# Kernel optimization log

Hardware: AMD Instinct MI355X
Metric: run time of the kernel (lower is better)

## Reference

```python
import jax, jax.numpy as jnp
import numpy as np
import math

D_MODEL = 1024
NHEAD = 16
D_HEAD = D_MODEL // NHEAD
TAU = 300.0
DELTA = 5.0 * 60.0  # delta_minutes -> seconds


def setup_inputs() -> dict:
    key = jax.random.key(0)
    ks = jax.random.split(key, 10)
    B, M = 4, 2048
    H = jax.random.normal(ks[0], (B, M, D_MODEL), dtype=jnp.float32)
    patch_mask = jax.random.randint(ks[1], (B, M), 0, 2).astype(jnp.int32)
    s = 1.0 / math.sqrt(D_MODEL)
    Wq = jax.random.normal(ks[2], (D_MODEL, D_MODEL), dtype=jnp.float32) * s
    bq = jnp.zeros((D_MODEL,), dtype=jnp.float32)
    Wk = jax.random.normal(ks[3], (D_MODEL, D_MODEL), dtype=jnp.float32) * s
    bk = jnp.zeros((D_MODEL,), dtype=jnp.float32)
    Wv = jax.random.normal(ks[4], (D_MODEL, D_MODEL), dtype=jnp.float32) * s
    bv = jnp.zeros((D_MODEL,), dtype=jnp.float32)
    Wo = jax.random.normal(ks[5], (D_MODEL, D_MODEL), dtype=jnp.float32) * s
    bo = jnp.zeros((D_MODEL,), dtype=jnp.float32)
    return {"H": H, "patch_mask": patch_mask, "Wq": Wq, "bq": bq,
            "Wk": Wk, "bk": bk, "Wv": Wv, "bv": bv, "Wo": Wo, "bo": bo}


def _time_bias(M):
    idx = jnp.arange(M)
    dist = jnp.abs(idx[:, None] - idx[None, :]).astype(jnp.float32) * DELTA
    w = jnp.exp(-dist / max(TAU, 1e-6))
    return jnp.log(w + 1e-12)  # (M, M)


def reference(H, patch_mask, Wq, bq, Wk, bk, Wv, bv, Wo, bo):
    B, M, D = H.shape
    nh, dh = NHEAD, D_HEAD
    # projections -> (B, nh, M, dh)
    q = (H @ Wq.T + bq).reshape(B, M, nh, dh).transpose(0, 2, 1, 3)
    k = (H @ Wk.T + bk).reshape(B, M, nh, dh).transpose(0, 2, 1, 3)
    v = (H @ Wv.T + bv).reshape(B, M, nh, dh).transpose(0, 2, 1, 3)
    attn = jnp.einsum('bhqd,bhkd->bhqk', q, k) / math.sqrt(dh)
    attn = attn + _time_bias(M)[None, None, :, :]
    key_pad = patch_mask <= 0  # (B, M)
    attn = jnp.where(key_pad[:, None, None, :], -1e9, attn)
    A = jax.nn.softmax(attn, axis=-1)
    out = jnp.einsum('bhqk,bhkd->bhqd', A, v)
    out = out.transpose(0, 2, 1, 3).reshape(B, M, D)
    out = out @ Wo.T + bo
    out = out * patch_mask[:, :, None].astype(out.dtype)
    return out
```

## Files before the change

### kernel.cpp

```cpp
#include <hip/hip_runtime.h>
#include <stdint.h>

typedef short short8 __attribute__((ext_vector_type(8)));
typedef float f32x4 __attribute__((ext_vector_type(4)));

#define B_    4
#define M_    2048
#define D_    1024
#define NH_   16
#define DH_   64
#define LOG2E 1.44269504f

__device__ __forceinline__ short f2bf(float f) {
  union { float f; uint32_t u; } v; v.f = f;
  uint32_t r = (v.u + 0x7fffu + ((v.u >> 16) & 1u)) >> 16;
  return (short)r;
}

__device__ __forceinline__ void gl_lds16(const void* g, void* l) {
  __builtin_amdgcn_global_load_lds(
      (__attribute__((address_space(1))) void*)(g),
      (__attribute__((address_space(3))) void*)(l),
      16, 0, 0);
}

__device__ __forceinline__ f32x4 mfma16(short8 a, short8 b, f32x4 c) {
  return __builtin_amdgcn_mfma_f32_16x16x32_bf16(a, b, c, 0, 0, 0);
}

__global__ __launch_bounds__(256) void cvt_all(const float* __restrict__ H,
                                               const float* __restrict__ s0,
                                               const float* __restrict__ s1,
                                               const float* __restrict__ s2,
                                               const float* __restrict__ s3,
                                               short* __restrict__ dH,
                                               short* __restrict__ d0,
                                               short* __restrict__ d1,
                                               short* __restrict__ d2,
                                               short* __restrict__ d3) {
  const int bidx = blockIdx.x;
  const float* src;
  short* dst;
  int i;
  if (bidx < 8192) {
    src = H; dst = dH; i = bidx * 256 + threadIdx.x;
  } else {
    const int y = (bidx - 8192) >> 10;
    src = (y == 0) ? s0 : (y == 1) ? s1 : (y == 2) ? s2 : s3;
    dst = (y == 0) ? d0 : (y == 1) ? d1 : (y == 2) ? d2 : d3;
    i = ((bidx - 8192) & 1023) * 256 + threadIdx.x;
  }
  float4 v = ((const float4*)src)[i];
  short4 o;
  o.x = f2bf(v.x); o.y = f2bf(v.y); o.z = f2bf(v.z); o.w = f2bf(v.w);
  ((short4*)dst)[i] = o;
}

__global__ __launch_bounds__(256, 3) void gemm_qkv(const short* __restrict__ A,
                                                   const short* __restrict__ Wqb,
                                                   const short* __restrict__ Wkb,
                                                   const short* __restrict__ Wvb,
                                                   const float* __restrict__ bq,
                                                   const float* __restrict__ bk,
                                                   const float* __restrict__ bv,
                                                   short* __restrict__ Qo,
                                                   short* __restrict__ Ko,
                                                   short* __restrict__ Vo) {
  __shared__ char smem_raw[34816];
  short* Abuf = (short*)smem_raw;
  short* Bbuf = (short*)smem_raw + 4096;

  const int L = blockIdx.x + 8 * (blockIdx.y + 64 * blockIdx.z);
  const int xcd = L & 7;
  const int s = L >> 3;
  const int m_local = s & 7;
  const int nz = s >> 3;
  const int nt = nz & 7, z = nz >> 3;
  const int m0 = (xcd * 8 + m_local) * 128;
  const int n0 = nt * 128;

  const short* Bt = (z == 0) ? Wqb : (z == 1) ? Wkb : Wvb;
  const float* bias = (z == 0) ? bq : (z == 1) ? bk : bv;
  const float scale = (z == 0) ? 0.125f : 1.0f;

  const int tid = threadIdx.x;
  const int w = tid >> 6, l = tid & 63;
  const int q4 = l >> 4, c = l & 15;
  const int wr = w >> 1, wc = w & 1;

  f32x4 acc[4][4] = {};
  const int arow = (l >> 2);
  const int acol = (l & 3) * 8;

  for (int kk = 0; kk < 32; ++kk) {
    const int k0 = kk * 32;
#pragma unroll
    for (int st = 0; st < 2; ++st) {
      const int chunk = w * 2 + st;
      gl_lds16(A + (size_t)(m0 + chunk * 16 + arow) * 1024 + k0 + acol,
               Abuf + chunk * 512);
      gl_lds16(Bt + (size_t)(n0 + chunk * 16 + arow) * 1024 + k0 + acol,
               Bbuf + chunk * 512);
    }
    __syncthreads();
    short8 af[4], bfr[4];
#pragma unroll
    for (int i = 0; i < 4; ++i)
      af[i] = *(const short8*)(Abuf + (wr * 64 + i * 16 + c) * 32 + q4 * 8);
#pragma unroll
    for (int j = 0; j < 4; ++j)
      bfr[j] = *(const short8*)(Bbuf + (wc * 64 + j * 16 + c) * 32 + q4 * 8);
#pragma unroll
    for (int i = 0; i < 4; ++i)
#pragma unroll
      for (int j = 0; j < 4; ++j)
        acc[i][j] = mfma16(af[i], bfr[j], acc[i][j]);
    __syncthreads();
  }

  if (z < 2) {
    short* Cb = (short*)smem_raw;
    short* out = (z == 0) ? Qo : Ko;
#pragma unroll
    for (int j = 0; j < 4; ++j) {
      const float bvv = bias[n0 + wc * 64 + j * 16 + c];
#pragma unroll
      for (int i = 0; i < 4; ++i)
#pragma unroll
        for (int r = 0; r < 4; ++r)
          Cb[(wr * 64 + i * 16 + q4 * 4 + r) * 136 + wc * 64 + j * 16 + c] =
              f2bf((acc[i][j][r] + bvv) * scale);
    }
    __syncthreads();
#pragma unroll
    for (int p = 0; p < 8; ++p) {
      const int g = p * 256 + tid;
      const int row = g >> 4, seg = g & 15;
      *(short8*)(out + (size_t)(m0 + row) * 1024 + n0 + seg * 8) =
          *(const short8*)(Cb + row * 136 + seg * 8);
    }
  } else {
    short* Cb = (short*)smem_raw;
#pragma unroll
    for (int j = 0; j < 4; ++j) {
      const float bvv = bias[n0 + wc * 64 + j * 16 + c];
#pragma unroll
      for (int i = 0; i < 4; ++i) {
        short4 pk;
        pk.x = f2bf(acc[i][j][0] + bvv);
        pk.y = f2bf(acc[i][j][1] + bvv);
        pk.z = f2bf(acc[i][j][2] + bvv);
        pk.w = f2bf(acc[i][j][3] + bvv);
        *(short4*)(Cb + (wc * 64 + j * 16 + c) * 136 + wr * 64 + i * 16 + q4 * 4) = pk;
      }
    }
    __syncthreads();
    const int bb = m0 >> 11;
    const int tokb = m0 & 2047;
#pragma unroll
    for (int p = 0; p < 8; ++p) {
      const int g = p * 256 + tid;
      const int col = g >> 4, rseg = g & 15;
      const int colg = n0 + col;
      const int hh = colg >> 6, dd = colg & 63;
      *(short8*)(Vo + ((size_t)(bb * NH_ + hh) * DH_ + dd) * M_ + tokb + rseg * 8) =
          *(const short8*)(Cb + col * 136 + rseg * 8);
    }
  }
}

__global__ __launch_bounds__(256, 3) void gemm_oproj(const short* __restrict__ A,
                                                     const short* __restrict__ Bt,
                                                     const float* __restrict__ bias,
                                                     const int* __restrict__ pmask,
                                                     float* __restrict__ outp) {
  __shared__ char smem_raw[34816];
  short* Abuf = (short*)smem_raw;
  short* Bbuf = (short*)smem_raw + 4096;

  const int L = blockIdx.x + 8 * blockIdx.y;
  const int xcd = L & 7;
  const int s = L >> 3;
  const int m_local = s & 7;
  const int nt = s >> 3;
  const int m0 = (xcd * 8 + m_local) * 128;
  const int n0 = nt * 128;

  const int tid = threadIdx.x;
  const int w = tid >> 6, l = tid & 63;
  const int q4 = l >> 4, c = l & 15;
  const int wr = w >> 1, wc = w & 1;

  f32x4 acc[4][4] = {};
  const int arow = (l >> 2);
  const int acol = (l & 3) * 8;

  for (int kk = 0; kk < 32; ++kk) {
    const int k0 = kk * 32;
#pragma unroll
    for (int st = 0; st < 2; ++st) {
      const int chunk = w * 2 + st;
      gl_lds16(A + (size_t)(m0 + chunk * 16 + arow) * 1024 + k0 + acol,
               Abuf + chunk * 512);
      gl_lds16(Bt + (size_t)(n0 + chunk * 16 + arow) * 1024 + k0 + acol,
               Bbuf + chunk * 512);
    }
    __syncthreads();
    short8 af[4], bfr[4];
#pragma unroll
    for (int i = 0; i < 4; ++i)
      af[i] = *(const short8*)(Abuf + (wr * 64 + i * 16 + c) * 32 + q4 * 8);
#pragma unroll
    for (int j = 0; j < 4; ++j)
      bfr[j] = *(const short8*)(Bbuf + (wc * 64 + j * 16 + c) * 32 + q4 * 8);
#pragma unroll
    for (int i = 0; i < 4; ++i)
#pragma unroll
      for (int j = 0; j < 4; ++j)
        acc[i][j] = mfma16(af[i], bfr[j], acc[i][j]);
    __syncthreads();
  }

  float* Cf = (float*)smem_raw;
#pragma unroll
  for (int half = 0; half < 2; ++half) {
    __syncthreads();
    if (wr == half) {
#pragma unroll
      for (int j = 0; j < 4; ++j) {
        const float bvv = bias[n0 + wc * 64 + j * 16 + c];
#pragma unroll
        for (int i = 0; i < 4; ++i)
#pragma unroll
          for (int r = 0; r < 4; ++r)
            Cf[(i * 16 + q4 * 4 + r) * 132 + wc * 64 + j * 16 + c] =
                acc[i][j][r] + bvv;
      }
    }
    __syncthreads();
#pragma unroll
    for (int p = 0; p < 8; ++p) {
      const int g = p * 256 + tid;
      const int row = g >> 5, seg = g & 31;
      const int rowg = m0 + half * 64 + row;
      const float mmv = (pmask[rowg] > 0) ? 1.0f : 0.0f;
      float4 v = *(const float4*)(Cf + row * 132 + seg * 4);
      v.x *= mmv; v.y *= mmv; v.z *= mmv; v.w *= mmv;
      *(float4*)(outp + (size_t)rowg * 1024 + n0 + seg * 4) = v;
    }
  }
}

__global__ __launch_bounds__(256) void attn_kernel(const short* __restrict__ Qb,
                                                   const short* __restrict__ Kb,
                                                   const short* __restrict__ Vtb,
                                                   const int* __restrict__ pmask,
                                                   short* __restrict__ Attb) {
  __shared__ char smem[20480];
  short* Qs = (short*)smem;
  short* Ks = (short*)(smem + 8192);
  short* Vs = (short*)(smem + 12288);
  short* Ps = (short*)(smem + 16384);

  const int tid = threadIdx.x;
  const int w = tid >> 6, l = tid & 63;
  const int q4 = l >> 4, c = l & 15;
  const int qt = blockIdx.x, h = blockIdx.y, b = blockIdx.z;
  const short* Qbase = Qb + (size_t)(b * M_ + qt * 64) * D_ + h * DH_;
  const short* Kbase = Kb + (size_t)(b * M_) * D_ + h * DH_;
  const short* Vbase = Vtb + (size_t)(b * NH_ + h) * DH_ * M_;
  const int qrow0 = qt * 64 + w * 16;

  const int jt0 = max(0, 2 * qt - 2);
  const int jt1 = min(M_ / 32 - 1, 2 * qt + 3);

#pragma unroll
  for (int p = 0; p < 2; ++p) {
    const int u = p * 256 + tid;
    const int kh = u >> 8, row = (u >> 2) & 63, ch = u & 3;
    gl_lds16(Qbase + (size_t)row * D_ + kh * 32 + ch * 8, (char*)Qs + u * 16);
  }
  {
    const int j0 = jt0 * 32;
    const int kh = tid >> 7, krow = (tid >> 2) & 31, ch = tid & 3;
    gl_lds16(Kbase + (size_t)(j0 + krow) * D_ + kh * 32 + ch * 8, (char*)Ks + tid * 16);
    const int vrow = tid >> 2;
    gl_lds16(Vbase + (size_t)vrow * M_ + j0 + ch * 8, (char*)Vs + tid * 16);
  }
  __syncthreads();

  short8 aq0 = *(const short8*)(Qs + (w * 16 + c) * 32 + q4 * 8);
  short8 aq1 = *(const short8*)(Qs + 2048 + (w * 16 + c) * 32 + q4 * 8);

  f32x4 o[4] = {};
  float lrun[4] = {0.f, 0.f, 0.f, 0.f};
  short* Pw = Ps + w * 512;

  for (int jt = jt0; jt <= jt1; ++jt) {
    const int j0 = jt * 32;
    short8 b00 = *(const short8*)(Ks + c * 32 + q4 * 8);
    short8 b10 = *(const short8*)(Ks + 1024 + c * 32 + q4 * 8);
    short8 b01 = *(const short8*)(Ks + (16 + c) * 32 + q4 * 8);
    short8 b11 = *(const short8*)(Ks + 1024 + (16 + c) * 32 + q4 * 8);
    f32x4 s0 = {}, s1 = {};
    s0 = mfma16(aq0, b00, s0);
    s0 = mfma16(aq1, b10, s0);
    s1 = mfma16(aq0, b01, s1);
    s1 = mfma16(aq1, b11, s1);

    const float w0m = (pmask[b * M_ + j0 + c] > 0) ? 1.f : 0.f;
    const float w1m = (pmask[b * M_ + j0 + 16 + c] > 0) ? 1.f : 0.f;

#pragma unroll
    for (int r = 0; r < 4; ++r) {
      const int qr = qrow0 + q4 * 4 + r;
      const float d0 = fminf(fabsf((float)(qr - (j0 + c))), 28.0f);
      const float d1 = fminf(fabsf((float)(qr - (j0 + 16 + c))), 28.0f);
      const float p0 = exp2f((s0[r] - d0) * LOG2E) * w0m;
      const float p1 = exp2f((s1[r] - d1) * LOG2E) * w1m;
      Pw[(q4 * 4 + r) * 32 + c] = f2bf(p0);
      Pw[(q4 * 4 + r) * 32 + 16 + c] = f2bf(p1);
      lrun[r] += p0 + p1;
    }
    short8 pa = *(const short8*)(Pw + c * 32 + q4 * 8);
#pragma unroll
    for (int f = 0; f < 4; ++f) {
      short8 bv = *(const short8*)(Vs + (f * 16 + c) * 32 + q4 * 8);
      o[f] = mfma16(pa, bv, o[f]);
    }

    if (jt < jt1) {
      __syncthreads();
      const int j0n = j0 + 32;
      const int kh = tid >> 7, krow = (tid >> 2) & 31, ch = tid & 3;
      gl_lds16(Kbase + (size_t)(j0n + krow) * D_ + kh * 32 + ch * 8,
               (char*)Ks + tid * 16);
      const int vrow = tid >> 2;
      gl_lds16(Vbase + (size_t)vrow * M_ + j0n + ch * 8, (char*)Vs + tid * 16);
      __syncthreads();
    }
  }

#pragma unroll
  for (int r = 0; r < 4; ++r) {
#pragma unroll
    for (int off = 1; off < 16; off <<= 1)
      lrun[r] += __shfl_xor(lrun[r], off);
  }

  __syncthreads();
  short* Cb = (short*)(smem + 8192);
#pragma unroll
  for (int r = 0; r < 4; ++r) {
    const float inv = 1.0f / lrun[r];
#pragma unroll
    for (int f = 0; f < 4; ++f)
      Cb[(w * 16 + q4 * 4 + r) * 72 + f * 16 + c] = f2bf(o[f][r] * inv);
  }
  __syncthreads();
#pragma unroll
  for (int p = 0; p < 2; ++p) {
    const int u = p * 256 + tid;
    const int row = u >> 3, seg = u & 7;
    *(short8*)(Attb + (size_t)(b * M_ + qt * 64 + row) * D_ + h * DH_ + seg * 8) =
        *(const short8*)(Cb + row * 72 + seg * 8);
  }
}

extern "C" void kernel_launch(void* const* d_in, const int* in_sizes, int n_in,
                              void* d_out, int out_size, void* d_ws, size_t ws_size,
                              hipStream_t stream) {
  const float* H     = (const float*)d_in[0];
  const int*   pmask = (const int*)d_in[1];
  const float* Wq    = (const float*)d_in[2];
  const float* bq    = (const float*)d_in[3];
  const float* Wk    = (const float*)d_in[4];
  const float* bk    = (const float*)d_in[5];
  const float* Wv    = (const float*)d_in[6];
  const float* bv    = (const float*)d_in[7];
  const float* Wo    = (const float*)d_in[8];
  const float* bo    = (const float*)d_in[9];
  float* out = (float*)d_out;
  char* ws = (char*)d_ws;

  short* Hb   = (short*)(ws);
  short* Attb = (short*)(ws);
  short* Wqb  = (short*)(ws + (16u << 20));
  short* Wkb  = (short*)(ws + (18u << 20));
  short* Wvb  = (short*)(ws + (20u << 20));
  short* Wob  = (short*)(ws + (22u << 20));
  short* Qb   = (short*)(ws + (24u << 20));
  short* Kb2  = (short*)(ws + (40u << 20));
  short* Vtb  = (short*)(ws + (56u << 20));

  cvt_all<<<8192 + 4096, 256, 0, stream>>>(H, Wq, Wk, Wv, Wo,
                                           Hb, Wqb, Wkb, Wvb, Wob);

  dim3 gq(8, 64, 3);
  gemm_qkv<<<gq, 256, 0, stream>>>(Hb, Wqb, Wkb, Wvb, bq, bk, bv, Qb, Kb2, Vtb);

  attn_kernel<<<dim3(M_ / 64, NH_, B_), 256, 0, stream>>>(Qb, Kb2, Vtb, pmask, Attb);

  gemm_oproj<<<dim3(8, 64), 256, 0, stream>>>(Attb, Wob, bo, pmask, out);
}
```

Before: 222.4 us.

## Double-buffer K/V in attention and narrow output-projection tiles to 128x64

The attention kernel now ping-pongs between two K/V LDS buffers. It prefetches the next tile before computing on the current one and needs only one barrier per iteration. Q fragments are loaded straight from global memory into registers instead of going through LDS. The output-projection GEMM switches from 128x128 to 128x64 tiles, which doubles the block count to 1024 and drops the occupancy hint. This is meant to improve load balance across CUs, at the cost of lower per-block reuse of the A tile.

```diff
diff --git a/kernel.cpp b/kernel.cpp
--- a/kernel.cpp
+++ b/kernel.cpp
@@ -169,29 +169,29 @@
   }
 }
 
-__global__ __launch_bounds__(256, 3) void gemm_oproj(const short* __restrict__ A,
-                                                     const short* __restrict__ Bt,
-                                                     const float* __restrict__ bias,
-                                                     const int* __restrict__ pmask,
-                                                     float* __restrict__ outp) {
-  __shared__ char smem_raw[34816];
-  short* Abuf = (short*)smem_raw;
-  short* Bbuf = (short*)smem_raw + 4096;
-
-  const int L = blockIdx.x + 8 * blockIdx.y;
+__global__ __launch_bounds__(256) void gemm_oproj(const short* __restrict__ A,
+                                                  const short* __restrict__ Bt,
+                                                  const float* __restrict__ bias,
+                                                  const int* __restrict__ pmask,
+                                                  float* __restrict__ outp) {
+  __shared__ char smem[17408];
+  short* Abuf = (short*)smem;
+  short* Bbuf = (short*)(smem + 8192);
+
+  const int L = blockIdx.x + 16 * blockIdx.y;
   const int xcd = L & 7;
   const int s = L >> 3;
   const int m_local = s & 7;
   const int nt = s >> 3;
   const int m0 = (xcd * 8 + m_local) * 128;
-  const int n0 = nt * 128;
+  const int n0 = nt * 64;
 
   const int tid = threadIdx.x;
   const int w = tid >> 6, l = tid & 63;
   const int q4 = l >> 4, c = l & 15;
   const int wr = w >> 1, wc = w & 1;
 
-  f32x4 acc[4][4] = {};
+  f32x4 acc[4][2] = {};
   const int arow = (l >> 2);
   const int acol = (l & 3) * 8;
 
@@ -202,49 +202,49 @@
       const int chunk = w * 2 + st;
       gl_lds16(A + (size_t)(m0 + chunk * 16 + arow) * 1024 + k0 + acol,
                Abuf + chunk * 512);
-      gl_lds16(Bt + (size_t)(n0 + chunk * 16 + arow) * 1024 + k0 + acol,
-               Bbuf + chunk * 512);
-    }
-    __syncthreads();
-    short8 af[4], bfr[4];
+    }
+    gl_lds16(Bt + (size_t)(n0 + w * 16 + arow) * 1024 + k0 + acol,
+             Bbuf + w * 512);
+    __syncthreads();
+    short8 af[4], bfr[2];
 #pragma unroll
     for (int i = 0; i < 4; ++i)
       af[i] = *(const short8*)(Abuf + (wr * 64 + i * 16 + c) * 32 + q4 * 8);
 #pragma unroll
-    for (int j = 0; j < 4; ++j)
-      bfr[j] = *(const short8*)(Bbuf + (wc * 64 + j * 16 + c) * 32 + q4 * 8);
+    for (int j = 0; j < 2; ++j)
+      bfr[j] = *(const short8*)(Bbuf + (wc * 32 + j * 16 + c) * 32 + q4 * 8);
 #pragma unroll
     for (int i = 0; i < 4; ++i)
 #pragma unroll
-      for (int j = 0; j < 4; ++j)
+      for (int j = 0; j < 2; ++j)
         acc[i][j] = mfma16(af[i], bfr[j], acc[i][j]);
     __syncthreads();
   }
 
-  float* Cf = (float*)smem_raw;
+  float* Cf = (float*)smem;
 #pragma unroll
   for (int half = 0; half < 2; ++half) {
     __syncthreads();
     if (wr == half) {
 #pragma unroll
-      for (int j = 0; j < 4; ++j) {
-        const float bvv = bias[n0 + wc * 64 + j * 16 + c];
+      for (int j = 0; j < 2; ++j) {
+        const float bvv = bias[n0 + wc * 32 + j * 16 + c];
 #pragma unroll
         for (int i = 0; i < 4; ++i)
 #pragma unroll
           for (int r = 0; r < 4; ++r)
-            Cf[(i * 16 + q4 * 4 + r) * 132 + wc * 64 + j * 16 + c] =
+            Cf[(i * 16 + q4 * 4 + r) * 68 + wc * 32 + j * 16 + c] =
                 acc[i][j][r] + bvv;
       }
     }
     __syncthreads();
 #pragma unroll
-    for (int p = 0; p < 8; ++p) {
+    for (int p = 0; p < 4; ++p) {
       const int g = p * 256 + tid;
-      const int row = g >> 5, seg = g & 31;
+      const int row = g >> 4, seg = g & 15;
       const int rowg = m0 + half * 64 + row;
       const float mmv = (pmask[rowg] > 0) ? 1.0f : 0.0f;
-      float4 v = *(const float4*)(Cf + row * 132 + seg * 4);
+      float4 v = *(const float4*)(Cf + row * 68 + seg * 4);
       v.x *= mmv; v.y *= mmv; v.z *= mmv; v.w *= mmv;
       *(float4*)(outp + (size_t)rowg * 1024 + n0 + seg * 4) = v;
     }
@@ -257,51 +257,57 @@
                                                    const int* __restrict__ pmask,
                                                    short* __restrict__ Attb) {
   __shared__ char smem[20480];
-  short* Qs = (short*)smem;
-  short* Ks = (short*)(smem + 8192);
-  short* Vs = (short*)(smem + 12288);
-  short* Ps = (short*)(smem + 16384);
+  short* Ks0 = (short*)smem;
+  short* Ks1 = (short*)(smem + 4096);
+  short* Vs0 = (short*)(smem + 8192);
+  short* Vs1 = (short*)(smem + 12288);
+  short* Ps  = (short*)(smem + 16384);
 
   const int tid = threadIdx.x;
   const int w = tid >> 6, l = tid & 63;
   const int q4 = l >> 4, c = l & 15;
   const int qt = blockIdx.x, h = blockIdx.y, b = blockIdx.z;
-  const short* Qbase = Qb + (size_t)(b * M_ + qt * 64) * D_ + h * DH_;
+  const short* Qrow = Qb + (size_t)(b * M_) * D_ + h * DH_;
   const short* Kbase = Kb + (size_t)(b * M_) * D_ + h * DH_;
   const short* Vbase = Vtb + (size_t)(b * NH_ + h) * DH_ * M_;
   const int qrow0 = qt * 64 + w * 16;
 
+  short8 aq0 = *(const short8*)(Qrow + (size_t)(qrow0 + c) * D_ + q4 * 8);
+  short8 aq1 = *(const short8*)(Qrow + (size_t)(qrow0 + c) * D_ + 32 + q4 * 8);
+
   const int jt0 = max(0, 2 * qt - 2);
   const int jt1 = min(M_ / 32 - 1, 2 * qt + 3);
 
-#pragma unroll
-  for (int p = 0; p < 2; ++p) {
-    const int u = p * 256 + tid;
-    const int kh = u >> 8, row = (u >> 2) & 63, ch = u & 3;
-    gl_lds16(Qbase + (size_t)row * D_ + kh * 32 + ch * 8, (char*)Qs + u * 16);
-  }
+  const int kh = tid >> 7, krow = (tid >> 2) & 31, ch = tid & 3;
+  const int vrow = tid >> 2;
+
   {
     const int j0 = jt0 * 32;
-    const int kh = tid >> 7, krow = (tid >> 2) & 31, ch = tid & 3;
-    gl_lds16(Kbase + (size_t)(j0 + krow) * D_ + kh * 32 + ch * 8, (char*)Ks + tid * 16);
-    const int vrow = tid >> 2;
-    gl_lds16(Vbase + (size_t)vrow * M_ + j0 + ch * 8, (char*)Vs + tid * 16);
+    gl_lds16(Kbase + (size_t)(j0 + krow) * D_ + kh * 32 + ch * 8, (char*)Ks0 + tid * 16);
+    gl_lds16(Vbase + (size_t)vrow * M_ + j0 + ch * 8, (char*)Vs0 + tid * 16);
   }
   __syncthreads();
-
-  short8 aq0 = *(const short8*)(Qs + (w * 16 + c) * 32 + q4 * 8);
-  short8 aq1 = *(const short8*)(Qs + 2048 + (w * 16 + c) * 32 + q4 * 8);
 
   f32x4 o[4] = {};
   float lrun[4] = {0.f, 0.f, 0.f, 0.f};
   short* Pw = Ps + w * 512;
 
   for (int jt = jt0; jt <= jt1; ++jt) {
+    const int buf = (jt - jt0) & 1;
     const int j0 = jt * 32;
-    short8 b00 = *(const short8*)(Ks + c * 32 + q4 * 8);
-    short8 b10 = *(const short8*)(Ks + 1024 + c * 32 + q4 * 8);
-    short8 b01 = *(const short8*)(Ks + (16 + c) * 32 + q4 * 8);
-    short8 b11 = *(const short8*)(Ks + 1024 + (16 + c) * 32 + q4 * 8);
+    if (jt < jt1) {
+      const int j0n = j0 + 32;
+      gl_lds16(Kbase + (size_t)(j0n + krow) * D_ + kh * 32 + ch * 8,
+               (char*)(buf ? Ks0 : Ks1) + tid * 16);
+      gl_lds16(Vbase + (size_t)vrow * M_ + j0n + ch * 8,
+               (char*)(buf ? Vs0 : Vs1) + tid * 16);
+    }
+    const short* Kt = buf ? Ks1 : Ks0;
+    const short* Vt = buf ? Vs1 : Vs0;
+    short8 b00 = *(const short8*)(Kt + c * 32 + q4 * 8);
+    short8 b10 = *(const short8*)(Kt + 1024 + c * 32 + q4 * 8);
+    short8 b01 = *(const short8*)(Kt + (16 + c) * 32 + q4 * 8);
+    short8 b11 = *(const short8*)(Kt + 1024 + (16 + c) * 32 + q4 * 8);
     f32x4 s0 = {}, s1 = {};
     s0 = mfma16(aq0, b00, s0);
     s0 = mfma16(aq1, b10, s0);
@@ -325,20 +331,10 @@
     short8 pa = *(const short8*)(Pw + c * 32 + q4 * 8);
 #pragma unroll
     for (int f = 0; f < 4; ++f) {
-      short8 bv = *(const short8*)(Vs + (f * 16 + c) * 32 + q4 * 8);
+      short8 bv = *(const short8*)(Vt + (f * 16 + c) * 32 + q4 * 8);
       o[f] = mfma16(pa, bv, o[f]);
     }
-
-    if (jt < jt1) {
-      __syncthreads();
-      const int j0n = j0 + 32;
-      const int kh = tid >> 7, krow = (tid >> 2) & 31, ch = tid & 3;
-      gl_lds16(Kbase + (size_t)(j0n + krow) * D_ + kh * 32 + ch * 8,
-               (char*)Ks + tid * 16);
-      const int vrow = tid >> 2;
-      gl_lds16(Vbase + (size_t)vrow * M_ + j0n + ch * 8, (char*)Vs + tid * 16);
-      __syncthreads();
-    }
+    __syncthreads();
   }
 
 #pragma unroll
@@ -348,8 +344,7 @@
       lrun[r] += __shfl_xor(lrun[r], off);
   }
 
-  __syncthreads();
-  short* Cb = (short*)(smem + 8192);
+  short* Cb = (short*)smem;
 #pragma unroll
   for (int r = 0; r < 4; ++r) {
     const float inv = 1.0f / lrun[r];
@@ -401,5 +396,5 @@
 
   attn_kernel<<<dim3(M_ / 64, NH_, B_), 256, 0, stream>>>(Qb, Kb2, Vtb, pmask, Attb);
 
-  gemm_oproj<<<dim3(8, 64), 256, 0, stream>>>(Attb, Wob, bo, pmask, out);
-}
+  gemm_oproj<<<dim3(16, 64), 256, 0, stream>>>(Attb, Wob, bo, pmask, out);
+}
```

New measurement: 222.1 us. No clear change (-0.1%).
